# Performance work log

Hardware: AMD Instinct MI355X
Metric: run time of the kernel (lower is better)

## Reference

```python
import jax, jax.numpy as jnp
import numpy as np

B, E, H, LEVELS, MAXN = 16, 256, 256, 12, 2
N = 2 ** LEVELS - 1  # 4095 nodes, level-order perfect binary tree
NODE_VOCAB, EDGE_VOCAB = 64, 128

PARAM_SHAPES = {
    'node_emb': (NODE_VOCAB, E), 'edge_emb': (EDGE_VOCAB, E),
    'bu_Wioux': (E, 3 * H), 'bu_bioux': (3 * H,), 'bu_Wfx': (E, H), 'bu_bfx': (H,),
    'bu_Wiouh': (MAXN * H, 3 * H), 'bu_Wfh': (MAXN, MAXN * H, H),
    'bu_eWih': (E, 4 * H), 'bu_eWhh': (H, 4 * H), 'bu_ebih': (4 * H,), 'bu_ebhh': (4 * H,),
    'td_Wioux': (E, 3 * H), 'td_bioux': (3 * H,), 'td_Wfx': (E, H), 'td_bfx': (H,),
    'td_Wiouhc': (MAXN * H, 3 * H), 'td_Wiouhp': (H, 3 * H),
    'td_Wfchild': (MAXN, (MAXN + 1) * H, H), 'td_Wfparent': ((MAXN + 1) * H, H),
    'td_eWih': (E, 4 * H), 'td_eWhh': (H, 4 * H), 'td_ebih': (4 * H,), 'td_ebhh': (4 * H,),
}
FLOAT_NAMES = list(PARAM_SHAPES)

_sig = jax.nn.sigmoid

def _lstm(x, h, c, Wih, Whh, bih, bhh):
    # torch nn.LSTMCell gate order: i, f, g, o
    g = x @ Wih + h @ Whh + bih + bhh
    i, f, gg, o = jnp.split(g, 4, axis=-1)
    c2 = _sig(f) * c + _sig(i) * jnp.tanh(gg)
    return _sig(o) * jnp.tanh(c2), c2

def _forward(p, node_ids, edge_ids):
    x_all = p['node_emb'][node_ids]  # [B,N,E]
    e_all = p['edge_emb'][edge_ids]  # [B,N,E] edge to parent
    bu_h = [None] * LEVELS
    bu_he = [None] * LEVELS
    bu_ce = [None] * LEVELS
    # ---- bottom-up n-ary TreeLSTM, level by level (deepest first) ----
    for l in range(LEVELS - 1, -1, -1):
        M = 2 ** l
        s = M - 1
        x = x_all[:, s:s + M]
        if l == LEVELS - 1:  # leaves: zero-padded children (no fc terms)
            ch_h = jnp.zeros((B, M, MAXN, H), x.dtype)
            ch_c = ch_h
        else:
            ch_h = bu_he[l + 1].reshape(B, M, MAXN, H)
            ch_c = bu_ce[l + 1].reshape(B, M, MAXN, H)
        cat = ch_h.reshape(B, M, MAXN * H)  # child_cat_h
        iou = x @ p['bu_Wioux'] + p['bu_bioux'] + cat @ p['bu_Wiouh']
        i, o, u = jnp.split(iou, 3, axis=-1)
        i, o, u = _sig(i), _sig(o), jnp.tanh(u)
        fx = x @ p['bu_Wfx'] + p['bu_bfx']
        f = _sig(fx[:, :, None, :] + jnp.einsum('bmc,kch->bmkh', cat, p['bu_Wfh']))
        c = i * u + (f * ch_c).sum(axis=2)
        h = o * jnp.tanh(c)
        bu_h[l] = h
        # edge-transition LSTMCell before passing state to parent
        he, ce = _lstm(e_all[:, s:s + M], h, c, p['bu_eWih'], p['bu_eWhh'], p['bu_ebih'], p['bu_ebhh'])
        bu_he[l] = he
        bu_ce[l] = ce
    # ---- top-down n-ary TreeLSTM (root first) ----
    td_h = [None] * LEVELS
    ph = jnp.zeros((B, 1, H), x_all.dtype)
    pc = ph
    for l in range(LEVELS):
        M = 2 ** l
        s = M - 1
        x = x_all[:, s:s + M]
        if l == LEVELS - 1:
            ch_h = jnp.zeros((B, M, MAXN, H), x.dtype)
            ch_c = ch_h
        else:
            ch_h = bu_he[l + 1].reshape(B, M, MAXN, H)
            ch_c = bu_ce[l + 1].reshape(B, M, MAXN, H)
        cat = ch_h.reshape(B, M, MAXN * H)
        iou = x @ p['td_Wioux'] + p['td_bioux'] + cat @ p['td_Wiouhc'] + ph @ p['td_Wiouhp']
        i, o, u = jnp.split(iou, 3, axis=-1)
        i, o, u = _sig(i), _sig(o), jnp.tanh(u)
        fx = x @ p['td_Wfx'] + p['td_bfx']
        pcat = jnp.concatenate([ph, cat], axis=-1)  # [B,M,(MAXN+1)H]
        f_ch = _sig(fx[:, :, None, :] + jnp.einsum('bmc,kch->bmkh', pcat, p['td_Wfchild']))
        f_par = _sig(fx + pcat @ p['td_Wfparent'])
        c = i * u + (f_ch * ch_c).sum(axis=2) + f_par * pc
        h = o * jnp.tanh(c)
        td_h[l] = h
        if l < LEVELS - 1:
            M2 = 2 * M
            s2 = 2 * M - 1
            ph_r = jnp.repeat(h, 2, axis=1)
            pc_r = jnp.repeat(c, 2, axis=1)
            ph, pc = _lstm(e_all[:, s2:s2 + M2], ph_r, pc_r, p['td_eWih'], p['td_eWhh'], p['td_ebih'], p['td_ebhh'])
    return jnp.concatenate([jnp.concatenate(bu_h, 1), jnp.concatenate(td_h, 1)], axis=-1)  # [B,N,2H]


def setup_inputs() -> dict:
    key = jax.random.key(0)
    ks = jax.random.split(key, len(PARAM_SHAPES) + 2)
    inp = {}
    for k, (name, shp) in zip(ks, PARAM_SHAPES.items()):
        inp[name] = jax.random.normal(k, shp, dtype=jnp.float32) * 0.05
    inp['node_ids'] = jax.random.randint(ks[-2], (B, N), 0, NODE_VOCAB)
    inp['edge_ids'] = jax.random.randint(ks[-1], (B, N), 0, EDGE_VOCAB)
    return inp


def reference(node_emb, edge_emb, bu_Wioux, bu_bioux, bu_Wfx, bu_bfx, bu_Wiouh, bu_Wfh,
              bu_eWih, bu_eWhh, bu_ebih, bu_ebhh, td_Wioux, td_bioux, td_Wfx, td_bfx,
              td_Wiouhc, td_Wiouhp, td_Wfchild, td_Wfparent, td_eWih, td_eWhh, td_ebih, td_ebhh,
              node_ids, edge_ids):
    floats = (node_emb, edge_emb, bu_Wioux, bu_bioux, bu_Wfx, bu_bfx, bu_Wiouh, bu_Wfh,
              bu_eWih, bu_eWhh, bu_ebih, bu_ebhh, td_Wioux, td_bioux, td_Wfx, td_bfx,
              td_Wiouhc, td_Wiouhp, td_Wfchild, td_Wfparent, td_eWih, td_eWhh, td_ebih, td_ebhh)
    return _forward(dict(zip(FLOAT_NAMES, floats)), node_ids, edge_ids)
```

## Files before the change

### kernel.cpp

```cpp
#include <hip/hip_runtime.h>
#include <math.h>

#define NB 16
#define NH 256
#define NLV 12
#define NN 4095
#define OUTW 512

typedef unsigned short u16;
typedef __attribute__((ext_vector_type(4))) float f32x4;
typedef __attribute__((ext_vector_type(8))) short bf16x8;

__device__ __forceinline__ float sigf(float x){
  return __fdividef(1.0f, 1.0f + __expf(-x));
}
__device__ __forceinline__ float tanh_fast(float x){
  return 1.0f - __fdividef(2.0f, 1.0f + __expf(2.0f * x));
}

__device__ __forceinline__ u16 f2bf(float x){
  unsigned int u = __float_as_uint(x);
  return (u16)((u + 0x7fffu + ((u >> 16) & 1u)) >> 16);
}
__device__ __forceinline__ float bf2f(u16 h){
  return __uint_as_float(((unsigned int)h) << 16);
}

__device__ __forceinline__ void gload16(const void* g, void* l){
  __builtin_amdgcn_global_load_lds(
      (const __attribute__((address_space(1))) unsigned int*)g,
      (__attribute__((address_space(3))) unsigned int*)l, 16, 0, 0);
}

template<int VAR, int NG>
__global__ __launch_bounds__(256, (NG >= 5 ? 3 : 4)) void fused_gemm(
    int R, int logM, int s,
    const int* __restrict__ ids,
    const u16* __restrict__ emb,
    const u16* __restrict__ hsrc,
    const u16* __restrict__ hsrc2,
    const u16* __restrict__ Wth, int wstride,
    const float* __restrict__ bias,
    const float* __restrict__ cce,
    const float* __restrict__ cprev,
    float* __restrict__ c_out,
    u16* __restrict__ h_out,
    float* __restrict__ out)
{
  constexpr int K0 = 256;
  constexpr int K1 = (VAR == 0) ? (NG == 5 ? 512 : 0) : 256;
  constexpr int K2 = (VAR == 2 && NG == 6) ? 512 : 0;
  constexpr int KTOT = K0 + K1 + K2;

  __shared__ u16 As[128][64];
  __shared__ u16 Bs[NG * 32][64];

  int bx = blockIdx.x;
  if ((gridDim.x & 7) == 0){
    int q = (int)gridDim.x >> 3;
    bx = (bx & 7) * q + (bx >> 3);
  }

  int tid = threadIdx.x, lane = tid & 63, w = tid >> 6;
  int wrow = w >> 1, whh = w & 1;
  int hh0 = blockIdx.y * 32;
  int M = 1 << logM;

  int lrow8 = lane >> 3;
  int gran  = lane & 7;
  int swz = (gran ^ lrow8) * 8;

  const u16* pa0[4]; const u16* pa1[4]; const u16* pa2[4];
  #pragma unroll
  for (int c = 0; c < 4; ++c){
    int gr = bx * 128 + c * 32 + w * 8 + lrow8;
    if (gr > R - 1) gr = R - 1;
    int b = gr >> logM, m = gr & (M - 1);
    int j = s + m;
    pa0[c] = emb + (size_t)ids[b * NN + j] * 256 + swz;
    if constexpr (K1 > 0){
      if constexpr (VAR == 0)
        pa1[c] = hsrc + ((size_t)(b * NN + 2 * j + 1)) * NH + swz;
      else if constexpr (VAR == 3)
        pa1[c] = hsrc + ((size_t)(b * (M >> 1) + (m >> 1))) * NH + swz;
      else
        pa1[c] = hsrc + (size_t)gr * NH + swz;
    }
    if constexpr (K2 > 0)
      pa2[c] = hsrc2 + ((size_t)(b * NN + 2 * j + 1)) * NH + swz;
  }
  const u16* pb = Wth + (size_t)(hh0 + w * 8 + lrow8) * wstride + swz;

  f32x4 acc[NG][4];
  #pragma unroll
  for (int g = 0; g < NG; ++g)
    #pragma unroll
    for (int i = 0; i < 4; ++i) acc[g][i] = (f32x4)0.0f;

  for (int kt = 0; kt < KTOT; kt += 64){
    __syncthreads();
    #pragma unroll
    for (int c = 0; c < 4; ++c){
      const u16* ga;
      if (kt < K0) ga = pa0[c] + kt;
      else if (K1 > 0 && kt < K0 + K1) ga = pa1[c] + (kt - K0);
      else ga = pa2[c] + (kt - K0 - K1);
      gload16(ga, &As[c * 32 + w * 8][0]);
    }
    #pragma unroll
    for (int g = 0; g < NG; ++g)
      gload16(pb + (size_t)g * 256 * wstride + kt, &Bs[g * 32 + w * 8][0]);
    __syncthreads();

    #pragma unroll
    for (int kc = 0; kc < 2; ++kc){
      int g2 = ((kc * 4 + (lane >> 4)) ^ (lane & 7)) * 8;
      bf16x8 a[4];
      #pragma unroll
      for (int i = 0; i < 4; ++i)
        a[i] = *(const bf16x8*)&As[wrow * 64 + i * 16 + (lane & 15)][g2];
      bf16x8 bf[NG];
      #pragma unroll
      for (int g = 0; g < NG; ++g)
        bf[g] = *(const bf16x8*)&Bs[g * 32 + whh * 16 + (lane & 15)][g2];
      #pragma unroll
      for (int g = 0; g < NG; ++g)
        #pragma unroll
        for (int i = 0; i < 4; ++i)
          acc[g][i] = __builtin_amdgcn_mfma_f32_16x16x32_bf16(a[i], bf[g], acc[g][i], 0, 0, 0);
    }
  }

  int hhL = hh0 + whh * 16 + (lane & 15);
  float bb[NG];
  #pragma unroll
  for (int g = 0; g < NG; ++g) bb[g] = bias[g * 256 + hhL];

  #pragma unroll
  for (int i = 0; i < 4; ++i){
    #pragma unroll
    for (int r = 0; r < 4; ++r){
      int row = bx * 128 + wrow * 64 + i * 16 + ((lane >> 4) << 2) + r;
      if (row >= R) continue;
      int b = row >> logM, m = row & (M - 1);
      int j = s + m;
      if constexpr (VAR == 0){
        float iv = sigf(acc[0][i][r] + bb[0]);
        float ov = sigf(acc[1][i][r] + bb[1]);
        float uv = tanh_fast(acc[2][i][r] + bb[2]);
        float c = iv * uv;
        if constexpr (NG == 5){
          float f0 = sigf(acc[3][i][r] + bb[3]);
          float f1 = sigf(acc[4][i][r] + bb[4]);
          c += f0 * cce[((size_t)(b * NN + 2 * j + 1)) * NH + hhL]
             + f1 * cce[((size_t)(b * NN + 2 * j + 2)) * NH + hhL];
        }
        float h = ov * tanh_fast(c);
        c_out[(size_t)row * NH + hhL] = c;
        h_out[(size_t)row * NH + hhL] = f2bf(h);
        out[((size_t)(b * NN + j)) * OUTW + hhL] = h;
      } else if constexpr (VAR == 1){
        float iv = sigf(acc[0][i][r] + bb[0]);
        float fv = sigf(acc[1][i][r] + bb[1]);
        float gg = tanh_fast(acc[2][i][r] + bb[2]);
        float ov = sigf(acc[3][i][r] + bb[3]);
        float c2 = fv * cprev[(size_t)row * NH + hhL] + iv * gg;
        float h2 = ov * tanh_fast(c2);
        size_t di = ((size_t)(b * NN + j)) * NH + hhL;
        h_out[di] = f2bf(h2);
        c_out[di] = c2;
      } else if constexpr (VAR == 2){
        float iv = sigf(acc[0][i][r] + bb[0]);
        float ov = sigf(acc[1][i][r] + bb[1]);
        float uv = tanh_fast(acc[2][i][r] + bb[2]);
        float fp = sigf(acc[3][i][r] + bb[3]);
        float c = iv * uv + fp * cprev[(size_t)row * NH + hhL];
        if constexpr (NG == 6){
          float f0 = sigf(acc[4][i][r] + bb[4]);
          float f1 = sigf(acc[5][i][r] + bb[5]);
          c += f0 * cce[((size_t)(b * NN + 2 * j + 1)) * NH + hhL]
             + f1 * cce[((size_t)(b * NN + 2 * j + 2)) * NH + hhL];
        }
        float h = ov * tanh_fast(c);
        c_out[(size_t)row * NH + hhL] = c;
        h_out[(size_t)row * NH + hhL] = f2bf(h);
        out[((size_t)(b * NN + j)) * OUTW + NH + hhL] = h;
      } else {
        float iv = sigf(acc[0][i][r] + bb[0]);
        float fv = sigf(acc[1][i][r] + bb[1]);
        float gg = tanh_fast(acc[2][i][r] + bb[2]);
        float ov = sigf(acc[3][i][r] + bb[3]);
        int par = b * (M >> 1) + (m >> 1);
        float c2 = fv * cprev[(size_t)par * NH + hhL] + iv * gg;
        float h2 = ov * tanh_fast(c2);
        h_out[(size_t)row * NH + hhL] = f2bf(h2);
        c_out[(size_t)row * NH + hhL] = c2;
      }
    }
  }
}


__global__ void pack_bu_node_t(const float* __restrict__ Wioux, const float* __restrict__ Wiouh,
                               const float* __restrict__ Wfx, const float* __restrict__ Wfh,
                               const float* __restrict__ bioux, const float* __restrict__ bfx,
                               u16* __restrict__ Wth, float* __restrict__ bd)
{
  int tid = blockIdx.x*256 + threadIdx.x;
  if (tid < 768*1280){
    int n = tid / 768, k = tid % 768;
    float v;
    if (n < 768){
      v = (k < 256) ? Wioux[k*768 + n] : Wiouh[(k-256)*768 + n];
    } else {
      int kidx = (n < 1024) ? 0 : 1;
      int nn = n - 768 - kidx*256;
      v = (k < 256) ? Wfx[k*256 + nn] : Wfh[((size_t)kidx*512 + (k-256))*256 + nn];
    }
    Wth[tid] = f2bf(v);
  }
  if (tid < 1280) bd[tid] = (tid < 768) ? bioux[tid] : bfx[(tid-768) & 255];
}

__global__ void pack_edge_t(const float* __restrict__ Wih, const float* __restrict__ Whh,
                            const float* __restrict__ bih, const float* __restrict__ bhh,
                            u16* __restrict__ Wth, float* __restrict__ bd)
{
  int tid = blockIdx.x*256 + threadIdx.x;
  if (tid < 512*1024){
    int n = tid / 512, k = tid % 512;
    float v = (k < 256) ? Wih[k*1024 + n] : Whh[(k-256)*1024 + n];
    Wth[tid] = f2bf(v);
  }
  if (tid < 1024) bd[tid] = bih[tid] + bhh[tid];
}

__global__ void pack_td_node_t(const float* __restrict__ Wioux, const float* __restrict__ Wiouhc,
                               const float* __restrict__ Wiouhp, const float* __restrict__ Wfx,
                               const float* __restrict__ Wfchild, const float* __restrict__ Wfparent,
                               const float* __restrict__ bioux, const float* __restrict__ bfx,
                               u16* __restrict__ Wth, float* __restrict__ bd)
{
  int tid = blockIdx.x*256 + threadIdx.x;
  if (tid < 1024*1536){
    int n = tid / 1024, k = tid % 1024;
    float v;
    if (n < 768){
      v = (k < 256) ? Wioux[k*768 + n]
        : (k < 512) ? Wiouhp[(k-256)*768 + n]
                    : Wiouhc[(k-512)*768 + n];
    } else if (n < 1024){
      int nn = n - 768;
      v = (k < 256) ? Wfx[k*256 + nn] : Wfparent[(size_t)(k-256)*256 + nn];
    } else {
      int kidx = (n < 1280) ? 0 : 1;
      int nn = n - 1024 - kidx*256;
      v = (k < 256) ? Wfx[k*256 + nn]
                    : Wfchild[((size_t)kidx*768 + (k-256))*256 + nn];
    }
    Wth[tid] = f2bf(v);
  }
  if (tid < 1536) bd[tid] = (tid < 768) ? bioux[tid] : bfx[(tid-768) & 255];
}

__global__ void pack_emb(const float* __restrict__ ne, const float* __restrict__ ee,
                         u16* __restrict__ neb, u16* __restrict__ eeb,
                         u16* __restrict__ ph_b, float* __restrict__ pc)
{
  int tid = blockIdx.x*256 + threadIdx.x;
  if (tid < 64*256)  neb[tid] = f2bf(ne[tid]);
  if (tid < 128*256) eeb[tid] = f2bf(ee[tid]);
  if (tid < NB*NH){ ph_b[tid] = 0; pc[tid] = 0.0f; }
}

extern "C" void kernel_launch(void* const* d_in, const int* in_sizes, int n_in,
                              void* d_out, int out_size, void* d_ws, size_t ws_size,
                              hipStream_t stream)
{
  const float* node_emb  = (const float*)d_in[0];
  const float* edge_emb  = (const float*)d_in[1];
  const float* bu_Wioux  = (const float*)d_in[2];
  const float* bu_bioux  = (const float*)d_in[3];
  const float* bu_Wfx    = (const float*)d_in[4];
  const float* bu_bfx    = (const float*)d_in[5];
  const float* bu_Wiouh  = (const float*)d_in[6];
  const float* bu_Wfh    = (const float*)d_in[7];
  const float* bu_eWih   = (const float*)d_in[8];
  const float* bu_eWhh   = (const float*)d_in[9];
  const float* bu_ebih   = (const float*)d_in[10];
  const float* bu_ebhh   = (const float*)d_in[11];
  const float* td_Wioux  = (const float*)d_in[12];
  const float* td_bioux  = (const float*)d_in[13];
  const float* td_Wfx    = (const float*)d_in[14];
  const float* td_bfx    = (const float*)d_in[15];
  const float* td_Wiouhc = (const float*)d_in[16];
  const float* td_Wiouhp = (const float*)d_in[17];
  const float* td_Wfchild= (const float*)d_in[18];
  const float* td_Wfparent=(const float*)d_in[19];
  const float* td_eWih   = (const float*)d_in[20];
  const float* td_eWhh   = (const float*)d_in[21];
  const float* td_ebih   = (const float*)d_in[22];
  const float* td_ebhh   = (const float*)d_in[23];
  const int* node_ids    = (const int*)d_in[24];
  const int* edge_ids    = (const int*)d_in[25];
  float* out = (float*)d_out;

  float* fw = (float*)d_ws;
  size_t fo = 0;
  float* bbun = fw + fo; fo += 1280;
  float* bbue = fw + fo; fo += 1024;
  float* btdn = fw + fo; fo += 1536;
  float* btde = fw + fo; fo += 1024;
  float* ce_all = fw + fo; fo += (size_t)NB*NN*NH;
  float* c_lvl  = fw + fo; fo += (size_t)NB*2048*NH;
  float* pc     = fw + fo; fo += (size_t)NB*2048*NH;

  u16* uw = (u16*)(fw + fo);
  size_t uo = 0;
  u16* Wbunh = uw + uo; uo += (size_t)768*1280;
  u16* Wbueh = uw + uo; uo += (size_t)512*1024;
  u16* Wtdnh = uw + uo; uo += (size_t)1024*1536;
  u16* Wtdeh = uw + uo; uo += (size_t)512*1024;
  u16* neb = uw + uo; uo += (size_t)64*256;
  u16* eeb = uw + uo; uo += (size_t)128*256;
  u16* he_b = uw + uo; uo += (size_t)NB*NN*NH;
  u16* hl_b = uw + uo; uo += (size_t)NB*2048*NH;
  u16* ph_b = uw + uo; uo += (size_t)NB*2048*NH;

  pack_bu_node_t<<<(768*1280+255)/256, 256, 0, stream>>>(bu_Wioux, bu_Wiouh, bu_Wfx, bu_Wfh,
      bu_bioux, bu_bfx, Wbunh, bbun);
  pack_edge_t<<<(512*1024+255)/256, 256, 0, stream>>>(bu_eWih, bu_eWhh, bu_ebih, bu_ebhh,
      Wbueh, bbue);
  pack_td_node_t<<<(1024*1536+255)/256, 256, 0, stream>>>(td_Wioux, td_Wiouhc, td_Wiouhp, td_Wfx,
      td_Wfchild, td_Wfparent, td_bioux, td_bfx, Wtdnh, btdn);
  pack_edge_t<<<(512*1024+255)/256, 256, 0, stream>>>(td_eWih, td_eWhh, td_ebih, td_ebhh,
      Wtdeh, btde);
  pack_emb<<<(128*256+255)/256, 256, 0, stream>>>(node_emb, edge_emb, neb, eeb, ph_b, pc);

  for (int l = NLV-1; l >= 0; --l){
    int M = 1<<l, s = M-1, R = NB*M;
    bool leaf = (l == NLV-1);
    dim3 grid((R + 127) / 128, NH / 32);
    if (leaf){
      fused_gemm<0,3><<<grid, 256, 0, stream>>>(R, l, s, node_ids,
          neb, neb, neb, Wbunh, 768, bbun,
          nullptr, nullptr, c_lvl, hl_b, out);
    } else {
      fused_gemm<0,5><<<grid, 256, 0, stream>>>(R, l, s, node_ids,
          neb, he_b, neb, Wbunh, 768, bbun,
          ce_all, nullptr, c_lvl, hl_b, out);
    }
    if (l > 0){
      fused_gemm<1,4><<<grid, 256, 0, stream>>>(R, l, s, edge_ids,
          eeb, hl_b, neb, Wbueh, 512, bbue,
          nullptr, c_lvl, ce_all, he_b, nullptr);
    }
  }

  for (int l = 0; l < NLV; ++l){
    int M = 1<<l, s = M-1, R = NB*M;
    bool leaf = (l == NLV-1);
    dim3 grid((R + 127) / 128, NH / 32);
    if (!leaf){
      fused_gemm<2,6><<<grid, 256, 0, stream>>>(R, l, s, node_ids,
          neb, ph_b, he_b, Wtdnh, 1024, btdn,
          ce_all, pc, c_lvl, hl_b, out);
      int M2 = 2*M, s2 = 2*M-1, R2 = NB*M2;
      dim3 grid2((R2 + 127) / 128, NH / 32);
      fused_gemm<3,4><<<grid2, 256, 0, stream>>>(R2, l+1, s2, edge_ids,
          eeb, hl_b, neb, Wtdeh, 512, btde,
          nullptr, c_lvl, pc, ph_b, nullptr);
    } else {
      fused_gemm<2,4><<<grid, 256, 0, stream>>>(R, l, s, node_ids,
          neb, ph_b, neb, Wtdnh, 1024, btdn,
          nullptr, pc, c_lvl, hl_b, out);
    }
  }
}
```

Before: 1.182 ms.

## Precompute embedding projections into per-vocab lookup tables and shortcut leaf level

Because node and edge inputs come from small vocabularies (64/128 ids), the x@W + bias terms are precomputed once per id into LUTs, and each fused GEMM starts its accumulators from a LUT gather instead of running the K=256 embedding slice through MFMA. The leaf level, which has zero children, becomes a per-id table computed once and gathered to all 32768 leaves, removing the leaf GEMM. This cuts about a quarter to a third of the MFMA K-loop work per launch, in exchange for strided scalar LUT loads at accumulator init and a few small extra kernels.

```diff
diff --git a/kernel.cpp b/kernel.cpp
--- a/kernel.cpp
+++ b/kernel.cpp
@@ -32,25 +32,23 @@
       (__attribute__((address_space(3))) unsigned int*)l, 16, 0, 0);
 }
 
-template<int VAR, int NG>
+template<int VAR, int NG, int LSTRIDE>
 __global__ __launch_bounds__(256, (NG >= 5 ? 3 : 4)) void fused_gemm(
     int R, int logM, int s,
     const int* __restrict__ ids,
-    const u16* __restrict__ emb,
+    const float* __restrict__ lut,
     const u16* __restrict__ hsrc,
     const u16* __restrict__ hsrc2,
     const u16* __restrict__ Wth, int wstride,
-    const float* __restrict__ bias,
     const float* __restrict__ cce,
     const float* __restrict__ cprev,
     float* __restrict__ c_out,
     u16* __restrict__ h_out,
     float* __restrict__ out)
 {
-  constexpr int K0 = 256;
-  constexpr int K1 = (VAR == 0) ? (NG == 5 ? 512 : 0) : 256;
+  constexpr int K1 = (VAR == 0) ? 512 : 256;
   constexpr int K2 = (VAR == 2 && NG == 6) ? 512 : 0;
-  constexpr int KTOT = K0 + K1 + K2;
+  constexpr int KTOT = K1 + K2;
 
   __shared__ u16 As[128][64];
   __shared__ u16 Bs[NG * 32][64];
@@ -70,46 +68,51 @@
   int gran  = lane & 7;
   int swz = (gran ^ lrow8) * 8;
 
-  const u16* pa0[4]; const u16* pa1[4]; const u16* pa2[4];
+  const u16* pa1[4]; const u16* pa2[4];
   #pragma unroll
   for (int c = 0; c < 4; ++c){
     int gr = bx * 128 + c * 32 + w * 8 + lrow8;
     if (gr > R - 1) gr = R - 1;
     int b = gr >> logM, m = gr & (M - 1);
     int j = s + m;
-    pa0[c] = emb + (size_t)ids[b * NN + j] * 256 + swz;
-    if constexpr (K1 > 0){
-      if constexpr (VAR == 0)
-        pa1[c] = hsrc + ((size_t)(b * NN + 2 * j + 1)) * NH + swz;
-      else if constexpr (VAR == 3)
-        pa1[c] = hsrc + ((size_t)(b * (M >> 1) + (m >> 1))) * NH + swz;
-      else
-        pa1[c] = hsrc + (size_t)gr * NH + swz;
-    }
+    if constexpr (VAR == 0)
+      pa1[c] = hsrc + ((size_t)(b * NN + 2 * j + 1)) * NH + swz;
+    else if constexpr (VAR == 3)
+      pa1[c] = hsrc + ((size_t)(b * (M >> 1) + (m >> 1))) * NH + swz;
+    else
+      pa1[c] = hsrc + (size_t)gr * NH + swz;
     if constexpr (K2 > 0)
       pa2[c] = hsrc2 + ((size_t)(b * NN + 2 * j + 1)) * NH + swz;
   }
   const u16* pb = Wth + (size_t)(hh0 + w * 8 + lrow8) * wstride + swz;
 
+  int hhL = hh0 + whh * 16 + (lane & 15);
   f32x4 acc[NG][4];
   #pragma unroll
-  for (int g = 0; g < NG; ++g)
-    #pragma unroll
-    for (int i = 0; i < 4; ++i) acc[g][i] = (f32x4)0.0f;
+  for (int i = 0; i < 4; ++i){
+    int rbase = bx * 128 + wrow * 64 + i * 16 + ((lane >> 4) << 2);
+    #pragma unroll
+    for (int r = 0; r < 4; ++r){
+      int row = rbase + r;
+      if (row > R - 1) row = R - 1;
+      int b = row >> logM, m = row & (M - 1);
+      int id = ids[b * NN + s + m];
+      const float* lp = lut + ((size_t)id * 256 + hhL) * LSTRIDE;
+      #pragma unroll
+      for (int g = 0; g < NG; ++g) acc[g][i][r] = lp[g];
+    }
+  }
 
   for (int kt = 0; kt < KTOT; kt += 64){
     __syncthreads();
     #pragma unroll
     for (int c = 0; c < 4; ++c){
-      const u16* ga;
-      if (kt < K0) ga = pa0[c] + kt;
-      else if (K1 > 0 && kt < K0 + K1) ga = pa1[c] + (kt - K0);
-      else ga = pa2[c] + (kt - K0 - K1);
+      const u16* ga = (kt < K1) ? pa1[c] + kt : pa2[c] + (kt - K1);
       gload16(ga, &As[c * 32 + w * 8][0]);
     }
     #pragma unroll
     for (int g = 0; g < NG; ++g)
-      gload16(pb + (size_t)g * 256 * wstride + kt, &Bs[g * 32 + w * 8][0]);
+      gload16(pb + 256 + (size_t)g * 256 * wstride + kt, &Bs[g * 32 + w * 8][0]);
     __syncthreads();
 
     #pragma unroll
@@ -131,11 +134,6 @@
     }
   }
 
-  int hhL = hh0 + whh * 16 + (lane & 15);
-  float bb[NG];
-  #pragma unroll
-  for (int g = 0; g < NG; ++g) bb[g] = bias[g * 256 + hhL];
-
   #pragma unroll
   for (int i = 0; i < 4; ++i){
     #pragma unroll
@@ -145,39 +143,37 @@
       int b = row >> logM, m = row & (M - 1);
       int j = s + m;
       if constexpr (VAR == 0){
-        float iv = sigf(acc[0][i][r] + bb[0]);
-        float ov = sigf(acc[1][i][r] + bb[1]);
-        float uv = tanh_fast(acc[2][i][r] + bb[2]);
+        float iv = sigf(acc[0][i][r]);
+        float ov = sigf(acc[1][i][r]);
+        float uv = tanh_fast(acc[2][i][r]);
         float c = iv * uv;
-        if constexpr (NG == 5){
-          float f0 = sigf(acc[3][i][r] + bb[3]);
-          float f1 = sigf(acc[4][i][r] + bb[4]);
-          c += f0 * cce[((size_t)(b * NN + 2 * j + 1)) * NH + hhL]
-             + f1 * cce[((size_t)(b * NN + 2 * j + 2)) * NH + hhL];
-        }
+        float f0 = sigf(acc[3][i][r]);
+        float f1 = sigf(acc[4 % NG][i][r]);
+        c += f0 * cce[((size_t)(b * NN + 2 * j + 1)) * NH + hhL]
+           + f1 * cce[((size_t)(b * NN + 2 * j + 2)) * NH + hhL];
         float h = ov * tanh_fast(c);
         c_out[(size_t)row * NH + hhL] = c;
         h_out[(size_t)row * NH + hhL] = f2bf(h);
         out[((size_t)(b * NN + j)) * OUTW + hhL] = h;
       } else if constexpr (VAR == 1){
-        float iv = sigf(acc[0][i][r] + bb[0]);
-        float fv = sigf(acc[1][i][r] + bb[1]);
-        float gg = tanh_fast(acc[2][i][r] + bb[2]);
-        float ov = sigf(acc[3][i][r] + bb[3]);
+        float iv = sigf(acc[0][i][r]);
+        float fv = sigf(acc[1][i][r]);
+        float gg = tanh_fast(acc[2][i][r]);
+        float ov = sigf(acc[3 % NG][i][r]);
         float c2 = fv * cprev[(size_t)row * NH + hhL] + iv * gg;
         float h2 = ov * tanh_fast(c2);
         size_t di = ((size_t)(b * NN + j)) * NH + hhL;
         h_out[di] = f2bf(h2);
         c_out[di] = c2;
       } else if constexpr (VAR == 2){
-        float iv = sigf(acc[0][i][r] + bb[0]);
-        float ov = sigf(acc[1][i][r] + bb[1]);
-        float uv = tanh_fast(acc[2][i][r] + bb[2]);
-        float fp = sigf(acc[3][i][r] + bb[3]);
+        float iv = sigf(acc[0][i][r]);
+        float ov = sigf(acc[1][i][r]);
+        float uv = tanh_fast(acc[2][i][r]);
+        float fp = sigf(acc[3 % NG][i][r]);
         float c = iv * uv + fp * cprev[(size_t)row * NH + hhL];
         if constexpr (NG == 6){
-          float f0 = sigf(acc[4][i][r] + bb[4]);
-          float f1 = sigf(acc[5][i][r] + bb[5]);
+          float f0 = sigf(acc[4 % NG][i][r]);
+          float f1 = sigf(acc[5 % NG][i][r]);
           c += f0 * cce[((size_t)(b * NN + 2 * j + 1)) * NH + hhL]
              + f1 * cce[((size_t)(b * NN + 2 * j + 2)) * NH + hhL];
         }
@@ -186,10 +182,10 @@
         h_out[(size_t)row * NH + hhL] = f2bf(h);
         out[((size_t)(b * NN + j)) * OUTW + NH + hhL] = h;
       } else {
-        float iv = sigf(acc[0][i][r] + bb[0]);
-        float fv = sigf(acc[1][i][r] + bb[1]);
-        float gg = tanh_fast(acc[2][i][r] + bb[2]);
-        float ov = sigf(acc[3][i][r] + bb[3]);
+        float iv = sigf(acc[0][i][r]);
+        float fv = sigf(acc[1][i][r]);
+        float gg = tanh_fast(acc[2][i][r]);
+        float ov = sigf(acc[3 % NG][i][r]);
         int par = b * (M >> 1) + (m >> 1);
         float c2 = fv * cprev[(size_t)par * NH + hhL] + iv * gg;
         float h2 = ov * tanh_fast(c2);
@@ -198,6 +194,59 @@
       }
     }
   }
+}
+
+__global__ void build_lut(int nids, int ncols, int stride,
+                          const u16* __restrict__ embb,
+                          const u16* __restrict__ Wt, int wstride,
+                          const float* __restrict__ bias,
+                          float* __restrict__ lut)
+{
+  int t = blockIdx.x * 256 + threadIdx.x;
+  if (t >= nids * ncols) return;
+  int id = t / ncols, n = t % ncols;
+  const u16* e  = embb + id * 256;
+  const u16* wv = Wt + (size_t)n * wstride;
+  float z = bias[n];
+  for (int k = 0; k < 256; k += 8){
+    #pragma unroll
+    for (int q = 0; q < 8; ++q)
+      z += bf2f(e[k + q]) * bf2f(wv[k + q]);
+  }
+  int hh = n & 255, g = n >> 8;
+  lut[((size_t)id * 256 + hh) * stride + g] = z;
+}
+
+__global__ void build_leaf(const float* __restrict__ lut_bun,
+                           float* __restrict__ c64, float* __restrict__ h64f,
+                           u16* __restrict__ h64b)
+{
+  int t = blockIdx.x * 256 + threadIdx.x;
+  const float* lp = lut_bun + (size_t)t * 5;
+  float iv = sigf(lp[0]), ov = sigf(lp[1]), uv = tanh_fast(lp[2]);
+  float c = iv * uv;
+  float h = ov * tanh_fast(c);
+  c64[t] = c; h64f[t] = h; h64b[t] = f2bf(h);
+}
+
+__global__ void leaf_gather(const int* __restrict__ node_ids,
+                            const float* __restrict__ c64,
+                            const float* __restrict__ h64f,
+                            const u16* __restrict__ h64b,
+                            float* __restrict__ c_lvl, u16* __restrict__ hl_b,
+                            float* __restrict__ out)
+{
+  int t = blockIdx.x * 256 + threadIdx.x;
+  int gr = t >> 6, q4 = (t & 63) << 2;
+  int b = gr >> 11, m = gr & 2047;
+  int j = 2047 + m;
+  int id = node_ids[b * NN + j];
+  float4 cv = *(const float4*)(c64 + id * 256 + q4);
+  float4 hv = *(const float4*)(h64f + id * 256 + q4);
+  uint2 hb  = *(const uint2*)(h64b + id * 256 + q4);
+  *(float4*)(c_lvl + (size_t)gr * 256 + q4) = cv;
+  *(uint2*)(hl_b + (size_t)gr * 256 + q4) = hb;
+  *(float4*)(out + ((size_t)(b * NN + j)) * OUTW + q4) = hv;
 }
 
 
@@ -311,6 +360,12 @@
   float* bbue = fw + fo; fo += 1024;
   float* btdn = fw + fo; fo += 1536;
   float* btde = fw + fo; fo += 1024;
+  float* lut_bun = fw + fo; fo += (size_t)64*256*5;
+  float* lut_tdn = fw + fo; fo += (size_t)64*256*6;
+  float* lut_bue = fw + fo; fo += (size_t)128*256*4;
+  float* lut_tde = fw + fo; fo += (size_t)128*256*4;
+  float* c64  = fw + fo; fo += (size_t)64*256;
+  float* h64f = fw + fo; fo += (size_t)64*256;
   float* ce_all = fw + fo; fo += (size_t)NB*NN*NH;
   float* c_lvl  = fw + fo; fo += (size_t)NB*2048*NH;
   float* pc     = fw + fo; fo += (size_t)NB*2048*NH;
@@ -323,6 +378,7 @@
   u16* Wtdeh = uw + uo; uo += (size_t)512*1024;
   u16* neb = uw + uo; uo += (size_t)64*256;
   u16* eeb = uw + uo; uo += (size_t)128*256;
+  u16* h64b = uw + uo; uo += (size_t)64*256;
   u16* he_b = uw + uo; uo += (size_t)NB*NN*NH;
   u16* hl_b = uw + uo; uo += (size_t)NB*2048*NH;
   u16* ph_b = uw + uo; uo += (size_t)NB*2048*NH;
@@ -337,23 +393,28 @@
       Wtdeh, btde);
   pack_emb<<<(128*256+255)/256, 256, 0, stream>>>(node_emb, edge_emb, neb, eeb, ph_b, pc);
 
-  for (int l = NLV-1; l >= 0; --l){
+  build_lut<<<(64*1280+255)/256, 256, 0, stream>>>(64, 1280, 5, neb, Wbunh, 768, bbun, lut_bun);
+  build_lut<<<(64*1536+255)/256, 256, 0, stream>>>(64, 1536, 6, neb, Wtdnh, 1024, btdn, lut_tdn);
+  build_lut<<<(128*1024+255)/256, 256, 0, stream>>>(128, 1024, 4, eeb, Wbueh, 512, bbue, lut_bue);
+  build_lut<<<(128*1024+255)/256, 256, 0, stream>>>(128, 1024, 4, eeb, Wtdeh, 512, btde, lut_tde);
+  build_leaf<<<64, 256, 0, stream>>>(lut_bun, c64, h64f, h64b);
+
+  {
+    int R = NB * 2048;
+    leaf_gather<<<(R * 64) / 256, 256, 0, stream>>>(node_ids, c64, h64f, h64b,
+        c_lvl, hl_b, out);
+    dim3 grid((R + 127) / 128, NH / 32);
+    fused_gemm<1,4,4><<<grid, 256, 0, stream>>>(R, 11, 2047, edge_ids,
+        lut_bue, hl_b, nullptr, Wbueh, 512, nullptr, c_lvl, ce_all, he_b, nullptr);
+  }
+  for (int l = NLV-2; l >= 0; --l){
     int M = 1<<l, s = M-1, R = NB*M;
-    bool leaf = (l == NLV-1);
     dim3 grid((R + 127) / 128, NH / 32);
-    if (leaf){
-      fused_gemm<0,3><<<grid, 256, 0, stream>>>(R, l, s, node_ids,
-          neb, neb, neb, Wbunh, 768, bbun,
-          nullptr, nullptr, c_lvl, hl_b, out);
-    } else {
-      fused_gemm<0,5><<<grid, 256, 0, stream>>>(R, l, s, node_ids,
-          neb, he_b, neb, Wbunh, 768, bbun,
-          ce_all, nullptr, c_lvl, hl_b, out);
-    }
+    fused_gemm<0,5,5><<<grid, 256, 0, stream>>>(R, l, s, node_ids,
+        lut_bun, he_b, nullptr, Wbunh, 768, ce_all, nullptr, c_lvl, hl_b, out);
     if (l > 0){
-      fused_gemm<1,4><<<grid, 256, 0, stream>>>(R, l, s, edge_ids,
-          eeb, hl_b, neb, Wbueh, 512, bbue,
-          nullptr, c_lvl, ce_all, he_b, nullptr);
+      fused_gemm<1,4,4><<<grid, 256, 0, stream>>>(R, l, s, edge_ids,
+          lut_bue, hl_b, nullptr, Wbueh, 512, nullptr, c_lvl, ce_all, he_b, nullptr);
     }
   }
 
@@ -362,18 +423,15 @@
     bool leaf = (l == NLV-1);
     dim3 grid((R + 127) / 128, NH / 32);
     if (!leaf){
-      fused_gemm<2,6><<<grid, 256, 0, stream>>>(R, l, s, node_ids,
-          neb, ph_b, he_b, Wtdnh, 1024, btdn,
-          ce_all, pc, c_lvl, hl_b, out);
+      fused_gemm<2,6,6><<<grid, 256, 0, stream>>>(R, l, s, node_ids,
+          lut_tdn, ph_b, he_b, Wtdnh, 1024, ce_all, pc, c_lvl, hl_b, out);
       int M2 = 2*M, s2 = 2*M-1, R2 = NB*M2;
       dim3 grid2((R2 + 127) / 128, NH / 32);
-      fused_gemm<3,4><<<grid2, 256, 0, stream>>>(R2, l+1, s2, edge_ids,
-          eeb, hl_b, neb, Wtdeh, 512, btde,
-          nullptr, c_lvl, pc, ph_b, nullptr);
+      fused_gemm<3,4,4><<<grid2, 256, 0, stream>>>(R2, l+1, s2, edge_ids,
+          lut_tde, hl_b, nullptr, Wtdeh, 512, nullptr, c_lvl, pc, ph_b, nullptr);
     } else {
-      fused_gemm<2,4><<<grid, 256, 0, stream>>>(R, l, s, node_ids,
-          neb, ph_b, neb, Wtdnh, 1024, btdn,
-          nullptr, pc, c_lvl, hl_b, out);
-    }
-  }
-}
+      fused_gemm<2,4,6><<<grid, 256, 0, stream>>>(R, l, s, node_ids,
+          lut_tdn, ph_b, nullptr, Wtdnh, 1024, nullptr, pc, c_lvl, hl_b, out);
+    }
+  }
+}
```

After: 1.301 ms. 1.1x slower.

## Precompute leaf-level TreeLSTM states per node vocab id and gather

Applied to the files above, without the earlier changes.

Leaf nodes have zero children, so their state depends only on node id. The change computes gates for all 64 vocab ids once (a small LUT matmul plus activation) and gathers per-leaf c/h instead of running a GEMM over 32768 leaf rows. This removes the largest-level bottom-up node GEMM, at the cost of a few small extra kernel launches and a gather pass that writes c, bf16 h and output.

```diff
diff --git a/kernel.cpp b/kernel.cpp
--- a/kernel.cpp
+++ b/kernel.cpp
@@ -201,6 +201,60 @@
 }
 
 
+__global__ void build_lut(int nids, int ncols, int stride,
+                          const u16* __restrict__ embb,
+                          const u16* __restrict__ Wt, int wstride,
+                          const float* __restrict__ bias,
+                          float* __restrict__ lut)
+{
+  int t = blockIdx.x * 256 + threadIdx.x;
+  if (t >= nids * ncols) return;
+  int id = t / ncols, n = t % ncols;
+  const u16* e  = embb + id * 256;
+  const u16* wv = Wt + (size_t)n * wstride;
+  float z = bias[n];
+  for (int k = 0; k < 256; k += 8){
+    #pragma unroll
+    for (int q = 0; q < 8; ++q)
+      z += bf2f(e[k + q]) * bf2f(wv[k + q]);
+  }
+  int hh = n & 255, g = n >> 8;
+  lut[((size_t)id * 256 + hh) * stride + g] = z;
+}
+
+__global__ void build_leaf(const float* __restrict__ lut64,
+                           float* __restrict__ c64, float* __restrict__ h64f,
+                           u16* __restrict__ h64b)
+{
+  int t = blockIdx.x * 256 + threadIdx.x;
+  const float* lp = lut64 + (size_t)t * 3;
+  float iv = sigf(lp[0]), ov = sigf(lp[1]), uv = tanh_fast(lp[2]);
+  float c = iv * uv;
+  float h = ov * tanh_fast(c);
+  c64[t] = c; h64f[t] = h; h64b[t] = f2bf(h);
+}
+
+__global__ void leaf_gather(const int* __restrict__ node_ids,
+                            const float* __restrict__ c64,
+                            const float* __restrict__ h64f,
+                            const u16* __restrict__ h64b,
+                            float* __restrict__ c_lvl, u16* __restrict__ hl_b,
+                            float* __restrict__ out)
+{
+  int t = blockIdx.x * 256 + threadIdx.x;
+  int gr = t >> 6, q4 = (t & 63) << 2;
+  int b = gr >> 11, m = gr & 2047;
+  int j = 2047 + m;
+  int id = node_ids[b * NN + j];
+  float4 cv = *(const float4*)(c64 + id * 256 + q4);
+  float4 hv = *(const float4*)(h64f + id * 256 + q4);
+  uint2 hb  = *(const uint2*)(h64b + id * 256 + q4);
+  *(float4*)(c_lvl + (size_t)gr * 256 + q4) = cv;
+  *(uint2*)(hl_b + (size_t)gr * 256 + q4) = hb;
+  *(float4*)(out + ((size_t)(b * NN + j)) * OUTW + q4) = hv;
+}
+
+
 __global__ void pack_bu_node_t(const float* __restrict__ Wioux, const float* __restrict__ Wiouh,
                                const float* __restrict__ Wfx, const float* __restrict__ Wfh,
                                const float* __restrict__ bioux, const float* __restrict__ bfx,
@@ -311,6 +365,9 @@
   float* bbue = fw + fo; fo += 1024;
   float* btdn = fw + fo; fo += 1536;
   float* btde = fw + fo; fo += 1024;
+  float* lut64 = fw + fo; fo += (size_t)64*256*3;
+  float* c64  = fw + fo; fo += (size_t)64*256;
+  float* h64f = fw + fo; fo += (size_t)64*256;
   float* ce_all = fw + fo; fo += (size_t)NB*NN*NH;
   float* c_lvl  = fw + fo; fo += (size_t)NB*2048*NH;
   float* pc     = fw + fo; fo += (size_t)NB*2048*NH;
@@ -323,6 +380,7 @@
   u16* Wtdeh = uw + uo; uo += (size_t)512*1024;
   u16* neb = uw + uo; uo += (size_t)64*256;
   u16* eeb = uw + uo; uo += (size_t)128*256;
+  u16* h64b = uw + uo; uo += (size_t)64*256;
   u16* he_b = uw + uo; uo += (size_t)NB*NN*NH;
   u16* hl_b = uw + uo; uo += (size_t)NB*2048*NH;
   u16* ph_b = uw + uo; uo += (size_t)NB*2048*NH;
@@ -337,19 +395,24 @@
       Wtdeh, btde);
   pack_emb<<<(128*256+255)/256, 256, 0, stream>>>(node_emb, edge_emb, neb, eeb, ph_b, pc);
 
-  for (int l = NLV-1; l >= 0; --l){
+  build_lut<<<(64*768+255)/256, 256, 0, stream>>>(64, 768, 3, neb, Wbunh, 768, bbun, lut64);
+  build_leaf<<<64, 256, 0, stream>>>(lut64, c64, h64f, h64b);
+
+  {
+    int R = NB * 2048;
+    leaf_gather<<<(R * 64) / 256, 256, 0, stream>>>(node_ids, c64, h64f, h64b,
+        c_lvl, hl_b, out);
+    dim3 grid((R + 127) / 128, NH / 32);
+    fused_gemm<1,4><<<grid, 256, 0, stream>>>(R, 11, 2047, edge_ids,
+        eeb, hl_b, neb, Wbueh, 512, bbue,
+        nullptr, c_lvl, ce_all, he_b, nullptr);
+  }
+  for (int l = NLV-2; l >= 0; --l){
     int M = 1<<l, s = M-1, R = NB*M;
-    bool leaf = (l == NLV-1);
     dim3 grid((R + 127) / 128, NH / 32);
-    if (leaf){
-      fused_gemm<0,3><<<grid, 256, 0, stream>>>(R, l, s, node_ids,
-          neb, neb, neb, Wbunh, 768, bbun,
-          nullptr, nullptr, c_lvl, hl_b, out);
-    } else {
-      fused_gemm<0,5><<<grid, 256, 0, stream>>>(R, l, s, node_ids,
-          neb, he_b, neb, Wbunh, 768, bbun,
-          ce_all, nullptr, c_lvl, hl_b, out);
-    }
+    fused_gemm<0,5><<<grid, 256, 0, stream>>>(R, l, s, node_ids,
+        neb, he_b, neb, Wbunh, 768, bbun,
+        ce_all, nullptr, c_lvl, hl_b, out);
     if (l > 0){
       fused_gemm<1,4><<<grid, 256, 0, stream>>>(R, l, s, edge_ids,
           eeb, hl_b, neb, Wbueh, 512, bbue,
```

After: 1.170 ms. No clear change (-1.0%).
